# Optimization experiments

Hardware: AMD Instinct MI355X
Metric: run time of the kernel (lower is better)

The kernel has to match this reference:

```python
import jax, jax.numpy as jnp
import numpy as np

N_HEADS = 16
EPS = 1e-12  # torch F.normalize eps


def srmsnorm(x):
    # F.normalize(x, dim=-1) * sqrt(dim)
    d = x.shape[-1]
    norm = jnp.sqrt(jnp.sum(x * x, axis=-1, keepdims=True))
    return x / jnp.maximum(norm, EPS) * jnp.sqrt(jnp.float32(d))


def setup_inputs() -> dict:
    key = jax.random.key(0)
    ks = jax.random.split(key, 7)
    B, S, D, F = 2, 2048, 1024, 4096
    x = jax.random.normal(ks[0], (B, S, D), dtype=jnp.float32)
    # xavier-uniform-ish scale for square weights
    lim = np.sqrt(6.0 / (D + D)).astype(np.float32)
    wq = jax.random.uniform(ks[1], (D, D), jnp.float32, -lim, lim)
    wk = jax.random.uniform(ks[2], (D, D), jnp.float32, -lim, lim)
    wv = jax.random.uniform(ks[3], (D, D), jnp.float32, -lim, lim)
    wo = jax.random.uniform(ks[4], (D, D), jnp.float32, -lim, lim)
    w_in = jax.random.normal(ks[5], (D, F), dtype=jnp.float32) * np.sqrt(2.0 / D).astype(np.float32)
    lim2 = np.sqrt(6.0 / (D + F)).astype(np.float32)
    w_out = jax.random.uniform(ks[6], (F, D), jnp.float32, -lim2, lim2)
    return {"x": x, "wq": wq, "wk": wk, "wv": wv, "wo": wo, "w_in": w_in, "w_out": w_out}


def attention(x, wq, wk, wv, wo):
    B, S, D = x.shape
    H = N_HEADS
    hd = D // H
    scale = hd ** -0.5
    q = (x @ wq).reshape(B, S, H, hd).transpose(0, 2, 1, 3)  # [B,H,S,hd]
    k = (x @ wk).reshape(B, S, H, hd).transpose(0, 2, 1, 3)
    v = (x @ wv).reshape(B, S, H, hd).transpose(0, 2, 1, 3)
    scores = jnp.einsum('bhqd,bhkd->bhqk', q, k) * scale  # [B,H,S,S]
    causal = jnp.tril(jnp.ones((S, S), dtype=bool))
    scores = jnp.where(causal, scores, jnp.float32(-jnp.inf))
    probs = jax.nn.softmax(scores, axis=-1)
    out = jnp.einsum('bhqk,bhkd->bhqd', probs, v)  # [B,H,S,hd]
    out = out.transpose(0, 2, 1, 3).reshape(B, S, D)
    return out @ wo


def reference(x, wq, wk, wv, wo, w_in, w_out):
    h = x + attention(srmsnorm(x), wq, wk, wv, wo)
    ff = jax.nn.gelu(srmsnorm(h) @ w_in, approximate=True) @ w_out
    return h + ff
```

## Files before the change

kernel.cpp:

```cpp
#include <hip/hip_runtime.h>
#include <math.h>

#define BB 2
#define SS 2048
#define DD 1024
#define FF 4096
#define HH 16
#define MM (BB * SS)

typedef __attribute__((ext_vector_type(8))) short short8v;
typedef __attribute__((ext_vector_type(4))) float float4v;
typedef __attribute__((ext_vector_type(4))) unsigned short ushort4v;
typedef __attribute__((ext_vector_type(8))) unsigned short ushort8v;
typedef unsigned short u16;
typedef unsigned int u32;

#define MFMA16(A_, B_, C_) __builtin_amdgcn_mfma_f32_16x16x32_bf16((A_), (B_), (C_), 0, 0, 0)

__device__ __forceinline__ u16 f2bf(float f) {
    u32 u = __float_as_uint(f);
    u += 0x7FFF + ((u >> 16) & 1);
    return (u16)(u >> 16);
}

__device__ __forceinline__ void async16(void* lds, const void* g) {
    __builtin_amdgcn_global_load_lds(
        (const __attribute__((address_space(1))) u32*)g,
        (__attribute__((address_space(3))) u32*)lds, 16, 0, 0);
}

__device__ __forceinline__ float gelu_f(float x) {
    float u = 0.7978845608028654f * x * (1.0f + 0.044715f * x * x);
    float e = exp2f(u * 2.8853900817779268f);
    float th = 1.0f - 2.0f / (e + 1.0f);
    return 0.5f * x * (1.0f + th);
}

__global__ __launch_bounds__(256) void srmsnorm_bf16(const float* __restrict__ in,
                                                     u16* __restrict__ out) {
    const int row = blockIdx.x, t = threadIdx.x;
    float4 a = reinterpret_cast<const float4*>(in + (size_t)row * DD)[t];
    float ss = a.x * a.x + a.y * a.y + a.z * a.z + a.w * a.w;
#pragma unroll
    for (int off = 32; off > 0; off >>= 1) ss += __shfl_xor(ss, off);
    __shared__ float red[4];
    if ((t & 63) == 0) red[t >> 6] = ss;
    __syncthreads();
    float tot = red[0] + red[1] + red[2] + red[3];
    float sc = 32.0f / fmaxf(sqrtf(tot), 1e-12f);
    ushort4v ov;
    ov[0] = f2bf(a.x * sc); ov[1] = f2bf(a.y * sc);
    ov[2] = f2bf(a.z * sc); ov[3] = f2bf(a.w * sc);
    *(ushort4v*)(out + (size_t)row * DD + t * 4) = ov;
}

__device__ __forceinline__ void trans_tile(const float* __restrict__ in,
                                           u16* __restrict__ out, int K, int N,
                                           int n0, int k0, int t, float (*T)[65]) {
#pragma unroll
    for (int i = 0; i < 4; ++i) {
        int r = i * 16 + (t >> 4), c4 = (t & 15) * 4;
        float4 v = *reinterpret_cast<const float4*>(in + (size_t)(k0 + r) * N + n0 + c4);
        T[r][c4 + 0] = v.x; T[r][c4 + 1] = v.y; T[r][c4 + 2] = v.z; T[r][c4 + 3] = v.w;
    }
    __syncthreads();
#pragma unroll
    for (int i = 0; i < 4; ++i) {
        int r = i * 16 + (t >> 4), c4 = (t & 15) * 4;
        ushort4v ov;
#pragma unroll
        for (int j = 0; j < 4; ++j) ov[j] = f2bf(T[c4 + j][r]);
        *(ushort4v*)(out + (size_t)(n0 + r) * K + k0 + c4) = ov;
    }
}

__global__ __launch_bounds__(256) void wtrans_all(const float* __restrict__ wq,
                                                  const float* __restrict__ wk,
                                                  const float* __restrict__ wv,
                                                  const float* __restrict__ wo,
                                                  const float* __restrict__ wi,
                                                  const float* __restrict__ wo2,
                                                  char* __restrict__ ws) {
    __shared__ float T[64][65];
    const int t = threadIdx.x;
    const size_t MB = 1024 * 1024;
    int id = blockIdx.x;
    if (id < 1024) {
        const int which = id >> 8, l = id & 255;
        const float* in = which == 0 ? wq : which == 1 ? wk : which == 2 ? wv : wo;
        u16* out = (u16*)(ws + (size_t)which * 2 * MB);
        trans_tile(in, out, 1024, 1024, (l & 15) * 64, (l >> 4) * 64, t, T);
    } else if (id < 2048) {
        const int l = id - 1024;
        trans_tile(wi, (u16*)(ws + 8 * MB), 1024, 4096,
                   (l & 63) * 64, (l >> 6) * 64, t, T);
    } else {
        const int l = id - 2048;
        trans_tile(wo2, (u16*)(ws + 16 * MB), 4096, 1024,
                   (l & 15) * 64, (l >> 4) * 64, t, T);
    }
}

__global__ __launch_bounds__(256) void vtrans(const u16* __restrict__ vb,
                                              u16* __restrict__ vt) {
    __shared__ u16 T[64][88];
    const int t = threadIdx.x;
    const int s0 = blockIdx.x * 64, bh = blockIdx.y;
    const int b = bh >> 4, h = bh & 15;
#pragma unroll
    for (int i = 0; i < 2; ++i) {
        int r = i * 32 + (t >> 3), c8 = (t & 7) * 8;
        *(ushort8v*)&T[r][c8] =
            *(const ushort8v*)(vb + (size_t)(b * SS + s0 + r) * DD + h * 64 + c8);
    }
    __syncthreads();
#pragma unroll
    for (int i = 0; i < 2; ++i) {
        int d = i * 32 + (t >> 3), s8 = (t & 7) * 8;
        ushort8v ov;
#pragma unroll
        for (int j = 0; j < 8; ++j) ov[j] = T[s8 + j][d];
        *(ushort8v*)(vt + ((size_t)bh * 64 + d) * SS + s0 + s8) = ov;
    }
}

template <int BM, int BN, int EPI>
__global__ __launch_bounds__(256) void gemm_bf16(const u16* __restrict__ A,
                                                 const u16* __restrict__ Bt,
                                                 const float* __restrict__ Res,
                                                 void* __restrict__ Cout,
                                                 int M, int N, int K) {
    __shared__ u16 As[BM * 32];
    __shared__ u16 Bs[BN * 32];
    constexpr int FM = BM / 32, FN = BN / 32;
    const int t = threadIdx.x;
    const int w = t >> 6, lane = t & 63;
    const int g = lane >> 4, c = lane & 15;
    const int wr = w >> 1, wc = w & 1;
    const int bm = blockIdx.y * BM, bn = blockIdx.x * BN;
    const int arow = t >> 2, au = (t & 3) * 8;

    float4v acc[FM][FN] = {};
    for (int k0 = 0; k0 < K; k0 += 32) {
        __syncthreads();
#pragma unroll
        for (int p = 0; p < BM / 64; ++p)
            async16(&As[(p * 64 + arow) * 32 + au],
                    A + (size_t)(bm + p * 64 + arow) * K + k0 + au);
#pragma unroll
        for (int p = 0; p < BN / 64; ++p)
            async16(&Bs[(p * 64 + arow) * 32 + au],
                    Bt + (size_t)(bn + p * 64 + arow) * K + k0 + au);
        __syncthreads();
        short8v af[FM], bf[FN];
#pragma unroll
        for (int mi = 0; mi < FM; ++mi)
            af[mi] = *(const short8v*)&As[(wr * (BM / 2) + mi * 16 + c) * 32 + g * 8];
#pragma unroll
        for (int ni = 0; ni < FN; ++ni)
            bf[ni] = *(const short8v*)&Bs[(wc * (BN / 2) + ni * 16 + c) * 32 + g * 8];
#pragma unroll
        for (int mi = 0; mi < FM; ++mi)
#pragma unroll
            for (int ni = 0; ni < FN; ++ni)
                acc[mi][ni] = MFMA16(af[mi], bf[ni], acc[mi][ni]);
    }
    const int row0 = bm + wr * (BM / 2), col0 = bn + wc * (BN / 2);
    if (EPI == 3) {
        const int seg = col0 >> 10, c0 = col0 & 1023;
        u16* dst = (u16*)Cout + (size_t)seg * ((size_t)MM * 1024);
#pragma unroll
        for (int mi = 0; mi < FM; ++mi)
#pragma unroll
            for (int r = 0; r < 4; ++r) {
                const size_t rw = (size_t)(row0 + mi * 16 + 4 * g + r) * 1024;
#pragma unroll
                for (int ni = 0; ni < FN; ++ni)
                    dst[rw + c0 + ni * 16 + c] = f2bf(acc[mi][ni][r]);
            }
        return;
    }
#pragma unroll
    for (int mi = 0; mi < FM; ++mi)
#pragma unroll
        for (int r = 0; r < 4; ++r) {
            const size_t rw = (size_t)(row0 + mi * 16 + 4 * g + r) * N;
#pragma unroll
            for (int ni = 0; ni < FN; ++ni) {
                const size_t off = rw + col0 + ni * 16 + c;
                float v = acc[mi][ni][r];
                if (EPI == 0)      ((u16*)Cout)[off] = f2bf(v);
                else if (EPI == 1) ((float*)Cout)[off] = v + Res[off];
                else               ((u16*)Cout)[off] = f2bf(gelu_f(v));
            }
        }
}

__global__ __launch_bounds__(64) void attn_mfma(const u16* __restrict__ Qb,
                                                const u16* __restrict__ Kb,
                                                const u16* __restrict__ Vt,
                                                u16* __restrict__ Ao) {
    __shared__ u16 Pl[2][16][88];
    const int lane = threadIdx.x;
    const int g = lane >> 4, c = lane & 15;
    const int bid = blockIdx.x;
    const int bh = bid & 31;
    const int u = 63 - (bid >> 5);
    const int b = bh >> 4, h = bh & 15;
    const int qrow0 = u * 32;
    const int ktmax = qrow0 >> 6;
    const size_t qkbase = (size_t)b * SS * DD + h * 64;
    const size_t vbase = (size_t)bh * 64 * SS;
    constexpr float SC = 0.18033688011112042f;

    short8v qf[2][2];
#pragma unroll
    for (int rb = 0; rb < 2; ++rb)
#pragma unroll
        for (int kh = 0; kh < 2; ++kh)
            qf[rb][kh] = *(const short8v*)(Qb + qkbase +
                             (size_t)(qrow0 + rb * 16 + c) * DD + kh * 32 + g * 8);

    float4v o[2][4] = {};
    float m_run[2][4], l_run[2][4];
#pragma unroll
    for (int rb = 0; rb < 2; ++rb)
#pragma unroll
        for (int r = 0; r < 4; ++r) { m_run[rb][r] = -1e30f; l_run[rb][r] = 0.0f; }

    for (int kt = 0; kt <= ktmax; ++kt) {
        short8v kf[4][2];
#pragma unroll
        for (int nb = 0; nb < 4; ++nb)
#pragma unroll
            for (int kh = 0; kh < 2; ++kh)
                kf[nb][kh] = *(const short8v*)(Kb + qkbase +
                                 (size_t)(kt * 64 + nb * 16 + c) * DD + kh * 32 + g * 8);
        float4v sa[2][4] = {};
        __builtin_amdgcn_s_setprio(1);
#pragma unroll
        for (int nb = 0; nb < 4; ++nb)
#pragma unroll
            for (int kh = 0; kh < 2; ++kh)
#pragma unroll
                for (int rb = 0; rb < 2; ++rb)
                    sa[rb][nb] = MFMA16(qf[rb][kh], kf[nb][kh], sa[rb][nb]);
        __builtin_amdgcn_s_setprio(0);

        const bool diag = (kt == ktmax);
#pragma unroll
        for (int rb = 0; rb < 2; ++rb)
#pragma unroll
            for (int nb = 0; nb < 4; ++nb)
#pragma unroll
                for (int r = 0; r < 4; ++r) {
                    float v = sa[rb][nb][r] * SC;
                    if (diag && (kt * 64 + nb * 16 + c > qrow0 + rb * 16 + 4 * g + r))
                        v = -3e38f;
                    sa[rb][nb][r] = v;
                }

#pragma unroll
        for (int rb = 0; rb < 2; ++rb) {
            float corr[4];
#pragma unroll
            for (int r = 0; r < 4; ++r) {
                float m0 = fmaxf(fmaxf(sa[rb][0][r], sa[rb][1][r]),
                                 fmaxf(sa[rb][2][r], sa[rb][3][r]));
                m0 = fmaxf(m0, __shfl_xor(m0, 1));
                m0 = fmaxf(m0, __shfl_xor(m0, 2));
                m0 = fmaxf(m0, __shfl_xor(m0, 4));
                m0 = fmaxf(m0, __shfl_xor(m0, 8));
                float mn = fmaxf(m_run[rb][r], m0);
                corr[r] = exp2f(m_run[rb][r] - mn);
                m_run[rb][r] = mn;
            }
#pragma unroll
            for (int nb = 0; nb < 4; ++nb)
#pragma unroll
                for (int r = 0; r < 4; ++r)
                    sa[rb][nb][r] = exp2f(sa[rb][nb][r] - m_run[rb][r]);
#pragma unroll
            for (int r = 0; r < 4; ++r) {
                float s_ = sa[rb][0][r] + sa[rb][1][r] + sa[rb][2][r] + sa[rb][3][r];
                s_ += __shfl_xor(s_, 1); s_ += __shfl_xor(s_, 2);
                s_ += __shfl_xor(s_, 4); s_ += __shfl_xor(s_, 8);
                l_run[rb][r] = l_run[rb][r] * corr[r] + s_;
            }
            float4v cv; cv[0] = corr[0]; cv[1] = corr[1]; cv[2] = corr[2]; cv[3] = corr[3];
#pragma unroll
            for (int nb = 0; nb < 4; ++nb) o[rb][nb] *= cv;
#pragma unroll
            for (int nb = 0; nb < 4; ++nb)
#pragma unroll
                for (int r = 0; r < 4; ++r)
                    Pl[rb][4 * g + r][nb * 16 + c] = f2bf(sa[rb][nb][r]);
        }

        short8v pa[2][2];
#pragma unroll
        for (int rb = 0; rb < 2; ++rb)
#pragma unroll
            for (int kh = 0; kh < 2; ++kh)
                pa[rb][kh] = *(const short8v*)&Pl[rb][c][kh * 32 + g * 8];
        short8v vf[4][2];
#pragma unroll
        for (int nb = 0; nb < 4; ++nb)
#pragma unroll
            for (int kh = 0; kh < 2; ++kh)
                vf[nb][kh] = *(const short8v*)(Vt + vbase +
                                 (size_t)(nb * 16 + c) * SS + kt * 64 + kh * 32 + g * 8);
        __builtin_amdgcn_s_setprio(1);
#pragma unroll
        for (int nb = 0; nb < 4; ++nb)
#pragma unroll
            for (int kh = 0; kh < 2; ++kh)
#pragma unroll
                for (int rb = 0; rb < 2; ++rb)
                    o[rb][nb] = MFMA16(pa[rb][kh], vf[nb][kh], o[rb][nb]);
        __builtin_amdgcn_s_setprio(0);
    }

#pragma unroll
    for (int rb = 0; rb < 2; ++rb) {
        float inv[4];
#pragma unroll
        for (int r = 0; r < 4; ++r) inv[r] = 1.0f / l_run[rb][r];
#pragma unroll
        for (int nb = 0; nb < 4; ++nb)
#pragma unroll
            for (int r = 0; r < 4; ++r)
                Ao[qkbase + (size_t)(qrow0 + rb * 16 + 4 * g + r) * DD + nb * 16 + c] =
                    f2bf(o[rb][nb][r] * inv[r]);
    }
}

extern "C" void kernel_launch(void* const* d_in, const int* in_sizes, int n_in,
                              void* d_out, int out_size, void* d_ws, size_t ws_size,
                              hipStream_t stream) {
    const float* x     = (const float*)d_in[0];
    const float* wq    = (const float*)d_in[1];
    const float* wk    = (const float*)d_in[2];
    const float* wv    = (const float*)d_in[3];
    const float* wo    = (const float*)d_in[4];
    const float* w_in  = (const float*)d_in[5];
    const float* w_out = (const float*)d_in[6];
    float* out = (float*)d_out;
    char* ws = (char*)d_ws;
    const size_t MB = 1024 * 1024;
    u16* wq_t  = (u16*)(ws + 0 * MB);
    u16* wo_t  = (u16*)(ws + 6 * MB);
    u16* wi_t  = (u16*)(ws + 8 * MB);
    u16* wo2_t = (u16*)(ws + 16 * MB);
    u16* xn    = (u16*)(ws + 24 * MB);
    u16* qb    = (u16*)(ws + 32 * MB);
    u16* vb    = (u16*)(ws + 48 * MB);
    u16* vt    = (u16*)(ws + 56 * MB);
    u16* ao    = (u16*)(ws + 64 * MB);
    u16* hn    = (u16*)(ws + 72 * MB);
    u16* gbuf  = (u16*)(ws + 80 * MB);

    dim3 blk(256);
    wtrans_all<<<dim3(3072), blk, 0, stream>>>(wq, wk, wv, wo, w_in, w_out, ws);

    srmsnorm_bf16<<<MM, blk, 0, stream>>>(x, xn);
    gemm_bf16<128, 128, 3><<<dim3(3072 / 128, MM / 128), blk, 0, stream>>>(
        xn, wq_t, nullptr, qb, MM, 3072, DD);
    vtrans<<<dim3(SS / 64, BB * HH), blk, 0, stream>>>(vb, vt);
    attn_mfma<<<dim3(32 * 64), dim3(64), 0, stream>>>(qb, qb + (size_t)MM * 1024, vt, ao);
    gemm_bf16<128, 128, 1><<<dim3(DD / 128, MM / 128), blk, 0, stream>>>(ao, wo_t, x, out, MM, DD, DD);
    srmsnorm_bf16<<<MM, blk, 0, stream>>>(out, hn);
    gemm_bf16<128, 128, 2><<<dim3(FF / 128, MM / 128), blk, 0, stream>>>(hn, wi_t, nullptr, gbuf, MM, FF, DD);
    gemm_bf16<128, 128, 1><<<dim3(DD / 128, MM / 128), blk, 0, stream>>>(gbuf, wo2_t, out, out, MM, DD, FF);
}
```

Baseline: 430.2 us.

## Split attention KV range across two blocks and remap GEMM tiles per XCD

Attention is split into two blocks per query tile, each covering half of the key tiles and writing unnormalized partial outputs plus running max and sum to workspace. A new combine kernel merges the two partials and writes the bf16 output. The aim is more parallelism and better load balance for the causal workload. The cost is an extra launch and a round trip of fp32 partials through memory. Separately, GEMM block IDs are remapped so consecutive tiles land on the same XCD, which should improve L2 locality.

New measurement: 418.5 us. -2.7%, faster.

```diff
diff --git a/kernel.cpp b/kernel.cpp
--- a/kernel.cpp
+++ b/kernel.cpp
@@ -137,7 +137,16 @@
     const int w = t >> 6, lane = t & 63;
     const int g = lane >> 4, c = lane & 15;
     const int wr = w >> 1, wc = w & 1;
-    const int bm = blockIdx.y * BM, bn = blockIdx.x * BN;
+    const int gx = gridDim.x;
+    const int nwg = gx * gridDim.y;
+    int wg = blockIdx.y * gx + blockIdx.x;
+    {
+        const int q = nwg >> 3, rr = nwg & 7;
+        const int xcd = wg & 7, loc = wg >> 3;
+        wg = (xcd < rr) ? xcd * (q + 1) + loc
+                        : rr * (q + 1) + (xcd - rr) * q + loc;
+    }
+    const int bm = (wg / gx) * BM, bn = (wg % gx) * BN;
     const int arow = t >> 2, au = (t & 3) * 8;
 
     float4v acc[FM][FN] = {};
@@ -196,19 +205,47 @@
         }
 }
 
-__global__ __launch_bounds__(64) void attn_mfma(const u16* __restrict__ Qb,
-                                                const u16* __restrict__ Kb,
-                                                const u16* __restrict__ Vt,
-                                                u16* __restrict__ Ao) {
+__global__ __launch_bounds__(64) void attn_split(const u16* __restrict__ Qb,
+                                                 const u16* __restrict__ Kb,
+                                                 const u16* __restrict__ Vt,
+                                                 float* __restrict__ po,
+                                                 float* __restrict__ pml) {
     __shared__ u16 Pl[2][16][88];
     const int lane = threadIdx.x;
     const int g = lane >> 4, c = lane & 15;
     const int bid = blockIdx.x;
-    const int bh = bid & 31;
-    const int u = 63 - (bid >> 5);
+    const int s = bid & 1;
+    const int uid = bid >> 1;
+    const int bh = uid & 31;
+    const int u = 63 - (uid >> 5);
     const int b = bh >> 4, h = bh & 15;
     const int qrow0 = u * 32;
-    const int ktmax = qrow0 >> 6;
+    const int nkt = (u >> 1) + 1;
+    const int half = (nkt + 1) >> 1;
+    const int kt0 = s ? half : 0;
+    const int kt1 = s ? nkt : half;
+    float* myo = po + ((size_t)(uid * 2 + s)) * 32 * 64;
+    float* mym = pml + ((size_t)(uid * 2 + s)) * 2 * 32;
+
+    if (kt0 >= kt1) {
+#pragma unroll
+        for (int rb = 0; rb < 2; ++rb)
+#pragma unroll
+            for (int nb = 0; nb < 4; ++nb)
+#pragma unroll
+                for (int r = 0; r < 4; ++r)
+                    myo[(rb * 16 + 4 * g + r) * 64 + nb * 16 + c] = 0.0f;
+        if (c == 0)
+#pragma unroll
+            for (int rb = 0; rb < 2; ++rb)
+#pragma unroll
+                for (int r = 0; r < 4; ++r) {
+                    mym[rb * 16 + 4 * g + r] = -1e30f;
+                    mym[32 + rb * 16 + 4 * g + r] = 0.0f;
+                }
+        return;
+    }
+
     const size_t qkbase = (size_t)b * SS * DD + h * 64;
     const size_t vbase = (size_t)bh * 64 * SS;
     constexpr float SC = 0.18033688011112042f;
@@ -228,7 +265,7 @@
 #pragma unroll
         for (int r = 0; r < 4; ++r) { m_run[rb][r] = -1e30f; l_run[rb][r] = 0.0f; }
 
-    for (int kt = 0; kt <= ktmax; ++kt) {
+    for (int kt = kt0; kt < kt1; ++kt) {
         short8v kf[4][2];
 #pragma unroll
         for (int nb = 0; nb < 4; ++nb)
@@ -247,7 +284,7 @@
                     sa[rb][nb] = MFMA16(qf[rb][kh], kf[nb][kh], sa[rb][nb]);
         __builtin_amdgcn_s_setprio(0);
 
-        const bool diag = (kt == ktmax);
+        const bool diag = (kt == nkt - 1);
 #pragma unroll
         for (int rb = 0; rb < 2; ++rb)
 #pragma unroll
@@ -322,17 +359,55 @@
     }
 
 #pragma unroll
-    for (int rb = 0; rb < 2; ++rb) {
-        float inv[4];
-#pragma unroll
-        for (int r = 0; r < 4; ++r) inv[r] = 1.0f / l_run[rb][r];
+    for (int rb = 0; rb < 2; ++rb)
 #pragma unroll
         for (int nb = 0; nb < 4; ++nb)
 #pragma unroll
             for (int r = 0; r < 4; ++r)
-                Ao[qkbase + (size_t)(qrow0 + rb * 16 + 4 * g + r) * DD + nb * 16 + c] =
-                    f2bf(o[rb][nb][r] * inv[r]);
-    }
+                myo[(rb * 16 + 4 * g + r) * 64 + nb * 16 + c] = o[rb][nb][r];
+    if (c == 0)
+#pragma unroll
+        for (int rb = 0; rb < 2; ++rb)
+#pragma unroll
+            for (int r = 0; r < 4; ++r) {
+                mym[rb * 16 + 4 * g + r] = m_run[rb][r];
+                mym[32 + rb * 16 + 4 * g + r] = l_run[rb][r];
+            }
+}
+
+__global__ __launch_bounds__(256) void attn_comb(const float* __restrict__ po,
+                                                 const float* __restrict__ pml,
+                                                 u16* __restrict__ Ao) {
+    const int uid = blockIdx.x;
+    const int bh = uid & 31;
+    const int u = 63 - (uid >> 5);
+    const int b = bh >> 4, h = bh & 15;
+    const int qrow0 = u * 32;
+    const int t = threadIdx.x;
+    const int row = t >> 3, c8 = (t & 7) * 8;
+
+    const float* ml0 = pml + (size_t)(uid * 2 + 0) * 64;
+    const float* ml1 = pml + (size_t)(uid * 2 + 1) * 64;
+    const float m0 = ml0[row], l0 = ml0[32 + row];
+    const float m1 = ml1[row], l1 = ml1[32 + row];
+    const float mm = fmaxf(m0, m1);
+    const float e0 = exp2f(m0 - mm), e1 = exp2f(m1 - mm);
+    const float inv = 1.0f / (e0 * l0 + e1 * l1);
+
+    const float* o0 = po + ((size_t)(uid * 2 + 0) * 32 + row) * 64 + c8;
+    const float* o1 = po + ((size_t)(uid * 2 + 1) * 32 + row) * 64 + c8;
+    float4 a0 = *(const float4*)o0, b0 = *(const float4*)(o0 + 4);
+    float4 a1 = *(const float4*)o1, b1 = *(const float4*)(o1 + 4);
+    ushort8v ov;
+    ov[0] = f2bf((e0 * a0.x + e1 * a1.x) * inv);
+    ov[1] = f2bf((e0 * a0.y + e1 * a1.y) * inv);
+    ov[2] = f2bf((e0 * a0.z + e1 * a1.z) * inv);
+    ov[3] = f2bf((e0 * a0.w + e1 * a1.w) * inv);
+    ov[4] = f2bf((e0 * b0.x + e1 * b1.x) * inv);
+    ov[5] = f2bf((e0 * b0.y + e1 * b1.y) * inv);
+    ov[6] = f2bf((e0 * b0.z + e1 * b1.z) * inv);
+    ov[7] = f2bf((e0 * b0.w + e1 * b1.w) * inv);
+    *(ushort8v*)(Ao + (size_t)b * SS * DD + (size_t)(qrow0 + row) * DD + h * 64 + c8) = ov;
 }
 
 extern "C" void kernel_launch(void* const* d_in, const int* in_sizes, int n_in,
@@ -359,6 +434,8 @@
     u16* ao    = (u16*)(ws + 64 * MB);
     u16* hn    = (u16*)(ws + 72 * MB);
     u16* gbuf  = (u16*)(ws + 80 * MB);
+    float* po  = (float*)(ws + 80 * MB);
+    float* pml = (float*)(ws + 24 * MB);
 
     dim3 blk(256);
     wtrans_all<<<dim3(3072), blk, 0, stream>>>(wq, wk, wv, wo, w_in, w_out, ws);
@@ -367,7 +444,9 @@
     gemm_bf16<128, 128, 3><<<dim3(3072 / 128, MM / 128), blk, 0, stream>>>(
         xn, wq_t, nullptr, qb, MM, 3072, DD);
     vtrans<<<dim3(SS / 64, BB * HH), blk, 0, stream>>>(vb, vt);
-    attn_mfma<<<dim3(32 * 64), dim3(64), 0, stream>>>(qb, qb + (size_t)MM * 1024, vt, ao);
+    attn_split<<<dim3(32 * 64 * 2), dim3(64), 0, stream>>>(
+        qb, qb + (size_t)MM * 1024, vt, po, pml);
+    attn_comb<<<dim3(2048), blk, 0, stream>>>(po, pml, ao);
     gemm_bf16<128, 128, 1><<<dim3(DD / 128, MM / 128), blk, 0, stream>>>(ao, wo_t, x, out, MM, DD, DD);
     srmsnorm_bf16<<<MM, blk, 0, stream>>>(out, hn);
     gemm_bf16<128, 128, 2><<<dim3(FF / 128, MM / 128), blk, 0, stream>>>(hn, wi_t, nullptr, gbuf, MM, FF, DD);
```
